# Performance work log

Hardware: AMD Instinct MI355X
Metric: run time of the kernel (lower is better)

The kernel has to match this reference:

```python
import jax, jax.numpy as jnp
import numpy as np
from jax import lax

BOS = 0
B, T, U = 8, 256, 64
IN, ENC_H, DEC_H, P, J, V = 80, 512, 512, 512, 512, 1024


def lstm_layer(x, Wih, Whh, b):
    """PyTorch-style LSTM layer. x: [B,T,I]; Wih: [4H,I]; Whh: [4H,H]; b: [4H]."""
    Bn = x.shape[0]
    H = Whh.shape[1]
    xp = jnp.einsum('bti,gi->btg', x, Wih) + b  # precompute input projections [B,T,4H]
    h0 = jnp.zeros((Bn, H), x.dtype)

    def step(carry, xt):
        h, c = carry
        g = xt + h @ Whh.T
        i, f, gg, o = jnp.split(g, 4, axis=-1)
        c = jax.nn.sigmoid(f) * c + jax.nn.sigmoid(i) * jnp.tanh(gg)
        h = jax.nn.sigmoid(o) * jnp.tanh(c)
        return (h, c), h

    _, hs = lax.scan(step, (h0, h0), xp.transpose(1, 0, 2))
    return hs.transpose(1, 0, 2)  # [B,T,H]


def setup_inputs() -> dict:
    key = jax.random.key(0)
    ks = jax.random.split(key, 20)
    s = 0.04  # ~1/sqrt(H) init scale
    inp = {
        'xs': jax.random.normal(ks[0], (B, T, IN), jnp.float32),
        'ys': jax.random.randint(ks[1], (B, U), 0, V),
        # encoder LSTM layer 0 / 1
        'enc_Wih0': jax.random.normal(ks[2], (4 * ENC_H, IN), jnp.float32) * s,
        'enc_Whh0': jax.random.normal(ks[3], (4 * ENC_H, ENC_H), jnp.float32) * s,
        'enc_b0': jnp.zeros((4 * ENC_H,), jnp.float32),
        'enc_Wih1': jax.random.normal(ks[4], (4 * ENC_H, ENC_H), jnp.float32) * s,
        'enc_Whh1': jax.random.normal(ks[5], (4 * ENC_H, ENC_H), jnp.float32) * s,
        'enc_b1': jnp.zeros((4 * ENC_H,), jnp.float32),
        'enc_projW': jax.random.normal(ks[6], (P, ENC_H), jnp.float32) * s,
        'enc_projb': jnp.zeros((P,), jnp.float32),
        # decoder
        'embed': jax.random.normal(ks[7], (V, DEC_H), jnp.float32) * s,
        'dec_Wih': jax.random.normal(ks[8], (4 * DEC_H, DEC_H), jnp.float32) * s,
        'dec_Whh': jax.random.normal(ks[9], (4 * DEC_H, DEC_H), jnp.float32) * s,
        'dec_b': jnp.zeros((4 * DEC_H,), jnp.float32),
        'dec_projW': jax.random.normal(ks[10], (P, DEC_H), jnp.float32) * s,
        'dec_projb': jnp.zeros((P,), jnp.float32),
        # joint MLP: Linear(2P -> J), Tanh, Linear(J -> V)
        'jW1': jax.random.normal(ks[11], (J, 2 * P), jnp.float32) * s,
        'jb1': jnp.zeros((J,), jnp.float32),
        'jW2': jax.random.normal(ks[12], (V, J), jnp.float32) * s,
        'jb2': jnp.zeros((V,), jnp.float32),
    }
    return inp


def reference(xs, ys, enc_Wih0, enc_Whh0, enc_b0, enc_Wih1, enc_Whh1, enc_b1,
              enc_projW, enc_projb, embed, dec_Wih, dec_Whh, dec_b,
              dec_projW, dec_projb, jW1, jb1, jW2, jb2):
    # Encoder: 2-layer LSTM + projection
    h = lstm_layer(xs, enc_Wih0, enc_Whh0, enc_b0)
    h = lstm_layer(h, enc_Wih1, enc_Whh1, enc_b1)
    h_enc = h @ enc_projW.T + enc_projb  # [B,T,P]

    # Decoder: BOS pad, embed, 1-layer LSTM + projection
    ys_p = jnp.pad(ys, ((0, 0), (1, 0)), constant_values=BOS)  # [B,U+1]
    e = embed[ys_p]
    hd = lstm_layer(e, dec_Wih, dec_Whh, dec_b)
    h_dec = hd @ dec_projW.T + dec_projb  # [B,U+1,P]

    # Joint: cat([h_enc,h_dec]) @ W1.T == h_enc @ W1[:,:P].T + h_dec @ W1[:,P:].T
    pre_enc = jnp.einsum('btp,jp->btj', h_enc, jW1[:, :P])
    pre_dec = jnp.einsum('bup,jp->buj', h_dec, jW1[:, P:])
    z = jnp.tanh(pre_enc[:, :, None, :] + pre_dec[:, None, :, :] + jb1)  # [B,T,U+1,J]
    logits = jnp.einsum('btuj,vj->btuv', z, jW2) + jb2  # [B,T,U+1,V]
    return logits
```

## Files before the change

### kernel.cpp

```cpp
#include <hip/hip_runtime.h>


typedef _Float16 f16;
typedef _Float16 f16x8 __attribute__((ext_vector_type(8)));
typedef float f32x4 __attribute__((ext_vector_type(4)));
using u32 = unsigned int;

#define BB   8
#define TT   256
#define UU1  65
#define HH   512
#define G4   2048
#define PP   512
#define JJ   512
#define VV   1024
#define SENT 0xFFFFFFFFu

#define LOADX(p)     __hip_atomic_load((p), __ATOMIC_RELAXED, __HIP_MEMORY_SCOPE_AGENT)
#define STOREX(p, v) __hip_atomic_store((p), (v), __ATOMIC_RELAXED, __HIP_MEMORY_SCOPE_AGENT)

static __device__ __forceinline__ u32 packf16(float a, float b) {
  f16 ha = (f16)a, hb = (f16)b;
  unsigned short ua = __builtin_bit_cast(unsigned short, ha);
  unsigned short ub = __builtin_bit_cast(unsigned short, hb);
  return (u32)ua | ((u32)ub << 16);
}
static __device__ __forceinline__ float sigm(float x) {
  x = fminf(30.f, fmaxf(-30.f, x));
  return __builtin_amdgcn_rcpf(1.f + __expf(-x));
}
static __device__ __forceinline__ float ftanh(float x) {
  x = fminf(15.f, fmaxf(-15.f, x));
  float t = __expf(2.f * x);
  return (t - 1.f) * __builtin_amdgcn_rcpf(t + 1.f);
}

__global__ void k_init(u32* __restrict__ p, int n, int z1, int z2) {
  int i = blockIdx.x * 256 + threadIdx.x;
  if (i >= n) return;
  bool z = (i < 2048) | ((u32)(i - z1) < 2048u) | ((u32)(i - z2) < 2048u);
  p[i] = z ? 0u : SENT;
}

struct CastSeg { const float* s; f16* d; int n4; };
struct CastArgs { CastSeg seg[10]; };
__global__ void k_cast_all(CastArgs a, int total4) {
  int i = blockIdx.x * 256 + threadIdx.x;
  if (i >= total4) return;
  int k = 0, off = i;
  while (off >= a.seg[k].n4) { off -= a.seg[k].n4; ++k; }
  const float4 v = *(const float4*)(a.seg[k].s + (size_t)off * 4);
  uint2 p; p.x = packf16(v.x, v.y); p.y = packf16(v.z, v.w);
  *(uint2*)(a.seg[k].d + (size_t)off * 4) = p;
}

__global__ void k_embed(const int* __restrict__ ys, const float* __restrict__ emb,
                        float* __restrict__ e) {
  int row = blockIdx.x;
  int b = row / UU1, u = row % UU1;
  int idx = (u == 0) ? 0 : ys[b * (UU1 - 1) + (u - 1)];
  const float4* s = (const float4*)(emb + (size_t)idx * HH);
  float4* d = (float4*)(e + (size_t)row * HH);
  d[threadIdx.x] = s[threadIdx.x];
}

__global__ void k_biasdot(const float* __restrict__ jW1, const float* __restrict__ encPb,
                          const float* __restrict__ dPb, const float* __restrict__ jb1,
                          float* __restrict__ bce, float* __restrict__ bcd) {
  int j = blockIdx.x * 256 + threadIdx.x;
  if (j >= 512) return;
  const float* rowE = jW1 + (size_t)j * 1024;
  const float* rowD = rowE + 512;
  float s1 = 0.f, s2 = 0.f;
  for (int p = 0; p < 512; p += 4) {
    float4 a = *(const float4*)(rowE + p), b = *(const float4*)(encPb + p);
    s1 += a.x * b.x + a.y * b.y + a.z * b.z + a.w * b.w;
    float4 c = *(const float4*)(rowD + p), d = *(const float4*)(dPb + p);
    s2 += c.x * d.x + c.y * d.y + c.z * d.z + c.w * d.w;
  }
  bce[j] = s1; bcd[j] = s2 + jb1[j];
}

__global__ __launch_bounds__(256) void k_gemm(
    const float* __restrict__ A, const f16* __restrict__ B,
    const float* __restrict__ bias, float* __restrict__ C,
    int M, int N, int K, int lda, int ldb) {
  __shared__ f16 As[128][72];
  __shared__ f16 Bs[128][72];
  int tid = threadIdx.x;
  int mb = blockIdx.y * 128, nb = blockIdx.x * 128;
  int wave = tid >> 6, lane = tid & 63;
  int wm = wave >> 1, wn = wave & 1;
  int rowa = lane & 15, kg = lane >> 4;
  f32x4 acc[4][4] = {};
  for (int k0 = 0; k0 < K; k0 += 64) {
    for (int idx = tid; idx < 2048; idx += 256) {
      int r = idx >> 4, cq = idx & 15;
      int gm = mb + r, gk = k0 + cq * 4;
      float4 v = make_float4(0.f, 0.f, 0.f, 0.f);
      if (gm < M && gk + 3 < K) v = *(const float4*)(A + (size_t)gm * lda + gk);
      uint2 p; p.x = packf16(v.x, v.y); p.y = packf16(v.z, v.w);
      *(uint2*)&As[r][cq * 4] = p;
    }
    for (int idx = tid; idx < 1024; idx += 256) {
      int r = idx >> 3, c8 = idx & 7;
      int gn = nb + r, gk = k0 + c8 * 8;
      uint4 v = make_uint4(0u, 0u, 0u, 0u);
      if (gn < N && gk + 7 < K) v = *(const uint4*)(B + (size_t)gn * ldb + gk);
      *(uint4*)&Bs[r][c8 * 8] = v;
    }
    __syncthreads();
#pragma unroll
    for (int kf = 0; kf < 2; ++kf) {
      f16x8 af[4], bf[4];
#pragma unroll
      for (int mt = 0; mt < 4; ++mt)
        af[mt] = *(const f16x8*)&As[wm * 64 + mt * 16 + rowa][kf * 32 + kg * 8];
#pragma unroll
      for (int nt = 0; nt < 4; ++nt)
        bf[nt] = *(const f16x8*)&Bs[wn * 64 + nt * 16 + rowa][kf * 32 + kg * 8];
#pragma unroll
      for (int mt = 0; mt < 4; ++mt)
#pragma unroll
        for (int nt = 0; nt < 4; ++nt)
          acc[mt][nt] = __builtin_amdgcn_mfma_f32_16x16x32_f16(af[mt], bf[nt], acc[mt][nt], 0, 0, 0);
    }
    __syncthreads();
  }
#pragma unroll
  for (int nt = 0; nt < 4; ++nt) {
    int gn = nb + wn * 64 + nt * 16 + rowa;
    float bv = bias ? bias[gn] : 0.f;
#pragma unroll
    for (int mt = 0; mt < 4; ++mt)
#pragma unroll
      for (int r = 0; r < 4; ++r) {
        int gm = mb + wm * 64 + mt * 16 + kg * 4 + r;
        if (gm < M) C[(size_t)gm * N + gn] = acc[mt][nt][r] + bv;
      }
  }
}

__global__ __launch_bounds__(256) void k_gemmT(
    const float* __restrict__ A, int lda, const f16* __restrict__ B2,
    f16* __restrict__ C16) {
  __shared__ f16 As[128][72];
  __shared__ f16 Bs[128][72];
  int tid = threadIdx.x;
  int mb = blockIdx.y * 128, nb = blockIdx.x * 128;
  int wave = tid >> 6, lane = tid & 63;
  int wm = wave >> 1, wn = wave & 1;
  int rowa = lane & 15, kg = lane >> 4;
  f32x4 acc[4][4] = {};
  for (int k0 = 0; k0 < 512; k0 += 64) {
    for (int idx = tid; idx < 2048; idx += 256) {
      int r = idx >> 4, cq = idx & 15;
      float4 v = *(const float4*)(A + (size_t)(mb + r) * lda + k0 + cq * 4);
      uint2 p; p.x = packf16(v.x, v.y); p.y = packf16(v.z, v.w);
      *(uint2*)&As[r][cq * 4] = p;
    }
    for (int idx = tid; idx < 1024; idx += 256) {
      int r = idx >> 4, c8 = idx & 15;
      uint4 v = *(const uint4*)(B2 + (size_t)(k0 + r) * 512 + nb + c8 * 8);
      f16 tmp[8]; *(uint4*)tmp = v;
#pragma unroll
      for (int e = 0; e < 8; ++e) Bs[c8 * 8 + e][r] = tmp[e];
    }
    __syncthreads();
#pragma unroll
    for (int kf = 0; kf < 2; ++kf) {
      f16x8 af[4], bf[4];
#pragma unroll
      for (int mt = 0; mt < 4; ++mt)
        af[mt] = *(const f16x8*)&As[wm * 64 + mt * 16 + rowa][kf * 32 + kg * 8];
#pragma unroll
      for (int nt = 0; nt < 4; ++nt)
        bf[nt] = *(const f16x8*)&Bs[wn * 64 + nt * 16 + rowa][kf * 32 + kg * 8];
#pragma unroll
      for (int mt = 0; mt < 4; ++mt)
#pragma unroll
        for (int nt = 0; nt < 4; ++nt)
          acc[mt][nt] = __builtin_amdgcn_mfma_f32_16x16x32_f16(af[mt], bf[nt], acc[mt][nt], 0, 0, 0);
    }
    __syncthreads();
  }
#pragma unroll
  for (int nt = 0; nt < 4; ++nt) {
    int gn = nb + wn * 64 + nt * 16 + rowa;
#pragma unroll
    for (int mt = 0; mt < 4; ++mt)
#pragma unroll
      for (int r = 0; r < 4; ++r) {
        int gm = mb + wm * 64 + mt * 16 + kg * 4 + r;
        C16[(size_t)gm * 512 + gn] = (f16)acc[mt][nt][r];
      }
  }
}

template <int NW>
static __device__ __forceinline__ void poll_batch(const u32* const* p, u32* vv) {
#pragma unroll
  for (int k = 0; k < NW; ++k) vv[k] = LOADX(p[k]);
  int gd = 0;
  while (++gd < (1 << 18)) {
    bool any = false;
#pragma unroll
    for (int k = 0; k < NW; ++k) any = any | (vv[k] == SENT);
    if (!any) break;
    __builtin_amdgcn_s_sleep(4);
#pragma unroll
    for (int k = 0; k < NW; ++k)
      if (vv[k] == SENT) vv[k] = LOADX(p[k]);
  }
}
static __device__ __forceinline__ void guard_spin(const u32* gp) {
  u32 v = LOADX(gp);
  int gd = 0;
  while (v == SENT && ++gd < (1 << 18)) {
    __builtin_amdgcn_s_sleep(2);
    v = LOADX(gp);
  }
}

static __device__ __forceinline__ void lstm_16(
    int wg, const float* __restrict__ xp, const f16* __restrict__ Whh,
    u32* __restrict__ hseq,
    float* __restrict__ hs, int S) {
  extern __shared__ char smem[];
  f16 (*W)[520] = (f16(*)[520])smem;
  f16 (*H)[520] = (f16(*)[520])(smem + 133120);
  float (*gat)[8][36] = (float(*)[8][36])(smem + 133120 + 8320);
  const int tid = threadIdx.x;
  const int u0 = wg * 32;
  const int wave = tid >> 6, lane = tid & 63;
  const int rowa = lane & 15, kg = lane >> 4;
  const int b = lane >> 3, ju = lane & 7;
  const int uglob = u0 + wave * 8 + ju;

  for (int idx = tid; idx < 128 * 64; idx += 256) {
    int r = idx >> 6, ck = idx & 63;
    int w = r >> 5, g = (r >> 3) & 3, u = r & 7;
    uint4 v = *(const uint4*)(Whh + ((size_t)(g * 512 + u0 + w * 8 + u)) * 512 + ck * 8);
    *(uint4*)&W[r][ck * 8] = v;
  }
  __syncthreads();

  float c = 0.f;
  for (int t = 0; t < S; ++t) {
    const u32* hb = hseq + (size_t)t * 2048;
    if (tid < 16) guard_spin(hb + tid * 16);
    __syncthreads();

    size_t xpo = ((size_t)b * S + t) * (size_t)G4 + uglob;
    float xi = xp[xpo], xf = xp[xpo + 512], xg = xp[xpo + 1024], xo = xp[xpo + 1536];

    const u32* ptr[8];
    u32 vv[8];
#pragma unroll
    for (int k = 0; k < 8; ++k) ptr[k] = hb + ((tid + k * 256) >> 8) * 256 + ((tid + k * 256) & 255);
    poll_batch<8>(ptr, vv);
#pragma unroll
    for (int k = 0; k < 8; ++k) {
      int idx = tid + k * 256;
      ((u32*)H)[(idx >> 8) * 260 + (idx & 255)] = vv[k];
    }
    __syncthreads();

    f32x4 acc0 = {0.f, 0.f, 0.f, 0.f}, acc1 = {0.f, 0.f, 0.f, 0.f};
#pragma unroll
    for (int kf = 0; kf < 16; ++kf) {
      f16x8 af = {};
      if (rowa < 8) af = *(const f16x8*)&H[rowa][kf * 32 + kg * 8];
      f16x8 b0 = *(const f16x8*)&W[wave * 32 + rowa][kf * 32 + kg * 8];
      f16x8 b1 = *(const f16x8*)&W[wave * 32 + 16 + rowa][kf * 32 + kg * 8];
      acc0 = __builtin_amdgcn_mfma_f32_16x16x32_f16(af, b0, acc0, 0, 0, 0);
      acc1 = __builtin_amdgcn_mfma_f32_16x16x32_f16(af, b1, acc1, 0, 0, 0);
    }
    if (kg < 2) {
#pragma unroll
      for (int r = 0; r < 4; ++r) {
        gat[wave][kg * 4 + r][rowa] = acc0[r];
        gat[wave][kg * 4 + r][16 + rowa] = acc1[r];
      }
    }
    float gi = gat[wave][b][ju] + xi;
    float gf = gat[wave][b][8 + ju] + xf;
    float gg = gat[wave][b][16 + ju] + xg;
    float go = gat[wave][b][24 + ju] + xo;
    c = sigm(gf) * c + sigm(gi) * ftanh(gg);
    float h = sigm(go) * ftanh(c);

    float hn = __shfl_down(h, 1);
    if ((ju & 1) == 0)
      STOREX(hseq + (size_t)(t + 1) * 2048 + ((b * 512 + uglob) >> 1), packf16(h, hn));
    if (hs) hs[((size_t)b * S + t) * HH + uglob] = h;
  }
}

static __device__ __forceinline__ void lstm_l1(
    int wg, const float* __restrict__ gb, const f16* __restrict__ Wih,
    const f16* __restrict__ Whh, const u32* __restrict__ hin,
    u32* __restrict__ hseq, float* __restrict__ hs, int S) {
  extern __shared__ char smem[];
  f16 (*W)[1032] = (f16(*)[1032])smem;
  f16 (*H)[1032] = (f16(*)[1032])(smem + 132096);
  float (*gat)[8][20] = (float(*)[8][20])(smem + 132096 + 16512);
  const int tid = threadIdx.x;
  const int u0 = wg * 16;
  const int wave = tid >> 6, lane = tid & 63;
  const int rowa = lane & 15, kg = lane >> 4;
  const int b = lane >> 2, ju = lane & 3;
  const int uglob = u0 + wave * 4 + ju;

  for (int idx = tid; idx < 64 * 64; idx += 256) {
    int r = idx >> 6, ck = idx & 63;
    int w = r >> 4, g = (r >> 2) & 3, u = r & 3;
    size_t grow = (size_t)(g * 512 + u0 + w * 4 + u) * 512;
    *(uint4*)&W[r][ck * 8]       = *(const uint4*)(Whh + grow + ck * 8);
    *(uint4*)&W[r][512 + ck * 8] = *(const uint4*)(Wih + grow + ck * 8);
  }
  float gbi = 0.f, gbf = 0.f, gbg = 0.f, gbo = 0.f;
  if (lane < 32) {
    gbi = gb[uglob]; gbf = gb[512 + uglob];
    gbg = gb[1024 + uglob]; gbo = gb[1536 + uglob];
  }
  __syncthreads();

  float c = 0.f;
  for (int t = 0; t < S; ++t) {
    const u32* hbS = hseq + (size_t)t * 2048;
    const u32* hbU = hin + (size_t)(t + 1) * 2048;
    if (tid < 32)       guard_spin(hbS + tid * 8);
    else if (tid < 48)  guard_spin(hbU + (tid - 32) * 16);
    __syncthreads();
    const u32* ptr[16];
    u32 vv[16];
#pragma unroll
    for (int k = 0; k < 8; ++k) {
      int idx = tid + k * 256;
      int r = idx >> 8, cu = idx & 255;
      ptr[k] = hbS + r * 256 + cu;
      ptr[k + 8] = hbU + r * 256 + cu;
    }
    poll_batch<16>(ptr, vv);
#pragma unroll
    for (int k = 0; k < 8; ++k) {
      int idx = tid + k * 256;
      int r = idx >> 8, cu = idx & 255;
      ((u32*)H)[r * 516 + cu] = vv[k];
      ((u32*)H)[r * 516 + 256 + cu] = vv[k + 8];
    }
    __syncthreads();

    f32x4 accA = {0.f, 0.f, 0.f, 0.f}, accB = {0.f, 0.f, 0.f, 0.f};
#pragma unroll
    for (int kf = 0; kf < 16; ++kf) {
      f16x8 afA = {}, afB = {};
      if (rowa < 8) {
        afA = *(const f16x8*)&H[rowa][kf * 32 + kg * 8];
        afB = *(const f16x8*)&H[rowa][(kf + 16) * 32 + kg * 8];
      }
      f16x8 bfA = *(const f16x8*)&W[wave * 16 + rowa][kf * 32 + kg * 8];
      f16x8 bfB = *(const f16x8*)&W[wave * 16 + rowa][(kf + 16) * 32 + kg * 8];
      accA = __builtin_amdgcn_mfma_f32_16x16x32_f16(afA, bfA, accA, 0, 0, 0);
      accB = __builtin_amdgcn_mfma_f32_16x16x32_f16(afB, bfB, accB, 0, 0, 0);
    }
    if (kg < 2) {
#pragma unroll
      for (int r = 0; r < 4; ++r) gat[wave][kg * 4 + r][rowa] = accA[r] + accB[r];
    }
    if (lane < 32) {
      float gi = gat[wave][b][ju]      + gbi;
      float gf = gat[wave][b][4 + ju]  + gbf;
      float gg = gat[wave][b][8 + ju]  + gbg;
      float go = gat[wave][b][12 + ju] + gbo;
      c = sigm(gf) * c + sigm(gi) * ftanh(gg);
      float h = sigm(go) * ftanh(c);
      float hn = __shfl_down(h, 1);
      if ((ju & 1) == 0)
        STOREX(hseq + (size_t)(t + 1) * 2048 + (b * 256 + (uglob >> 1)), packf16(h, hn));
      hs[((size_t)b * S + t) * HH + uglob] = h;
    }
  }
}

__global__ __launch_bounds__(256, 1) void k_lstm3(
    const float* xp0, const f16* Whh0, u32* hseq0,
    const float* b1, const f16* Wih1, const f16* Whh1, u32* hseq1, float* h1s,
    const float* xpd, const f16* Whhd, u32* hseqD, float* hds) {
  int g = blockIdx.x;
  if (g < 16)      lstm_16(g, xp0, Whh0, hseq0, nullptr, TT);
  else if (g < 48) lstm_l1(g - 16, b1, Wih1, Whh1, hseq0, hseq1, h1s, TT);
  else             lstm_16(g - 48, xpd, Whhd, hseqD, hds, UU1);
}

__global__ __launch_bounds__(512, 4) void k_joint(
    const float* __restrict__ pre_enc,
    const float* __restrict__ pre_dec,
    const f16* __restrict__ jW2,
    const float* __restrict__ jb2,
    float* __restrict__ out) {
  extern __shared__ char smem[];
  f16 (*Z)[520] = (f16(*)[520])smem;
  f16 (*Bs)[72] = (f16(*)[72])(smem + 66560);
  int tid = threadIdx.x;
  int m0 = blockIdx.x * 64;
  {
    int r = tid >> 3, q = tid & 7;
    int m = m0 + r;
    int bb = m / (TT * UU1);
    int rem = m % (TT * UU1);
    int t = rem / UU1, u = rem % UU1;
    const float* pe = pre_enc + ((size_t)bb * TT + t) * JJ + q * 64;
    const float* pd = pre_dec + ((size_t)bb * UU1 + u) * JJ + q * 64;
    for (int i = 0; i < 64; i += 8) {
      float4 e0 = *(const float4*)(pe + i);
      float4 e1 = *(const float4*)(pe + i + 4);
      float4 d0 = *(const float4*)(pd + i);
      float4 d1 = *(const float4*)(pd + i + 4);
      float z0 = ftanh(e0.x + d0.x), z1 = ftanh(e0.y + d0.y);
      float z2 = ftanh(e0.z + d0.z), z3 = ftanh(e0.w + d0.w);
      float z4 = ftanh(e1.x + d1.x), z5 = ftanh(e1.y + d1.y);
      float z6 = ftanh(e1.z + d1.z), z7 = ftanh(e1.w + d1.w);
      uint4 p; p.x = packf16(z0, z1); p.y = packf16(z2, z3);
      p.z = packf16(z4, z5); p.w = packf16(z6, z7);
      *(uint4*)&Z[r][q * 64 + i] = p;
    }
  }
  const int wave = tid >> 6, lane = tid & 63;
  const int wm = wave >> 2, wn = wave & 3;
  const int rowa = lane & 15, kg = lane >> 4;
  const int r8 = tid >> 3, c8 = tid & 7;

  uint4 nreg = *(const uint4*)(jW2 + (size_t)r8 * JJ + c8 * 8);

  f32x4 acc[2] = {};
  for (int it = 0; it < 128; ++it) {
    const int vc = it >> 3, ks = it & 7;
    __syncthreads();
    *(uint4*)&Bs[r8][c8 * 8] = nreg;
    if (it < 127) {
      int nvc = (it + 1) >> 3, nks = (it + 1) & 7;
      nreg = *(const uint4*)(jW2 + (size_t)(nvc * 64 + r8) * JJ + nks * 64 + c8 * 8);
    }
    __syncthreads();
#pragma unroll
    for (int kf = 0; kf < 2; ++kf) {
      int zo = ks * 64 + kf * 32 + kg * 8;
      f16x8 af  = *(const f16x8*)&Bs[wn * 16 + rowa][kf * 32 + kg * 8];
      f16x8 bf0 = *(const f16x8*)&Z[wm * 32 + rowa][zo];
      f16x8 bf1 = *(const f16x8*)&Z[wm * 32 + 16 + rowa][zo];
      acc[0] = __builtin_amdgcn_mfma_f32_16x16x32_f16(af, bf0, acc[0], 0, 0, 0);
      acc[1] = __builtin_amdgcn_mfma_f32_16x16x32_f16(af, bf1, acc[1], 0, 0, 0);
    }
    if (ks == 7) {
      int v = vc * 64 + wn * 16 + kg * 4;
      float4 bv = *(const float4*)(jb2 + v);
#pragma unroll
      for (int mt = 0; mt < 2; ++mt) {
        int m = m0 + wm * 32 + mt * 16 + rowa;
        f32x4 st;
        st[0] = acc[mt][0] + bv.x;
        st[1] = acc[mt][1] + bv.y;
        st[2] = acc[mt][2] + bv.z;
        st[3] = acc[mt][3] + bv.w;
        __builtin_nontemporal_store(st, (f32x4*)(out + (size_t)m * VV + v));
        acc[mt] = (f32x4){0.f, 0.f, 0.f, 0.f};
      }
    }
  }
}

extern "C" void kernel_launch(void* const* d_in, const int* in_sizes, int n_in,
                              void* d_out, int out_size, void* d_ws, size_t ws_size,
                              hipStream_t stream) {
  const float* xs    = (const float*)d_in[0];
  const int*   ys    = (const int*)d_in[1];
  const float* Wih0  = (const float*)d_in[2];
  const float* Whh0  = (const float*)d_in[3];
  const float* b0    = (const float*)d_in[4];
  const float* Wih1  = (const float*)d_in[5];
  const float* Whh1  = (const float*)d_in[6];
  const float* b1    = (const float*)d_in[7];
  const float* encPW = (const float*)d_in[8];
  const float* encPb = (const float*)d_in[9];
  const float* embed = (const float*)d_in[10];
  const float* dWih  = (const float*)d_in[11];
  const float* dWhh  = (const float*)d_in[12];
  const float* db    = (const float*)d_in[13];
  const float* dPW   = (const float*)d_in[14];
  const float* dPb   = (const float*)d_in[15];
  const float* jW1   = (const float*)d_in[16];
  const float* jb1   = (const float*)d_in[17];
  const float* jW2   = (const float*)d_in[18];
  const float* jb2   = (const float*)d_in[19];
  float* out = (float*)d_out;

  char* base = (char*)d_ws;
  size_t off = 0;
  auto alc = [&](size_t bytes) -> char* {
    char* p = base + off;
    off = (off + bytes + 255) & ~(size_t)255;
    return p;
  };
  f16* Wih0h = (f16*)alc((size_t)2048 * 80 * 2);
  f16* Whh0h = (f16*)alc((size_t)2048 * 512 * 2);
  f16* Wih1h = (f16*)alc((size_t)2048 * 512 * 2);
  f16* Whh1h = (f16*)alc((size_t)2048 * 512 * 2);
  f16* dWihh = (f16*)alc((size_t)2048 * 512 * 2);
  f16* dWhhh = (f16*)alc((size_t)2048 * 512 * 2);
  f16* ePWh  = (f16*)alc((size_t)512 * 512 * 2);
  f16* dPWh  = (f16*)alc((size_t)512 * 512 * 2);
  f16* jW2h  = (f16*)alc((size_t)1024 * 512 * 2);
  f16* Wceh  = (f16*)alc((size_t)512 * 512 * 2);
  f16* Wcdh  = (f16*)alc((size_t)512 * 512 * 2);
  float* bce  = (float*)alc((size_t)512 * 4);
  float* bcd  = (float*)alc((size_t)512 * 4);
  float* e    = (float*)alc((size_t)520 * 512 * 4);
  float* xp0  = (float*)alc((size_t)2048 * 2048 * 4);
  float* xpd  = (float*)alc((size_t)520 * 2048 * 4);
  float* h1s  = (float*)alc((size_t)2048 * 512 * 4);
  float* hds  = (float*)alc((size_t)520 * 512 * 4);
  float* penc = (float*)alc((size_t)2048 * 512 * 4);
  float* pdec = (float*)alc((size_t)520 * 512 * 4);
  u32* hseq0 = (u32*)alc((size_t)(TT + 1) * 2048 * 4);
  u32* hseq1 = (u32*)alc((size_t)(TT + 1) * 2048 * 4);
  u32* hseqD = (u32*)alc((size_t)(UU1 + 1) * 2048 * 4);
  if (off > ws_size) return;

  {
    int n = (int)(((TT + 1) * 2 + (UU1 + 1)) * 2048);
    int z1 = (int)(hseq1 - hseq0), z2 = (int)(hseqD - hseq0);
    k_init<<<dim3((n + 255) / 256), dim3(256), 0, stream>>>(hseq0, n, z1, z2);
  }
  {
    CastArgs ca = {};
    auto seg = [&](int i, const float* s, f16* d, size_t n) {
      ca.seg[i].s = s; ca.seg[i].d = d; ca.seg[i].n4 = (int)(n / 4);
    };
    seg(0, Wih0, Wih0h, (size_t)2048 * 80);
    seg(1, Whh0, Whh0h, (size_t)2048 * 512);
    seg(2, Wih1, Wih1h, (size_t)2048 * 512);
    seg(3, Whh1, Whh1h, (size_t)2048 * 512);
    seg(4, dWih, dWihh, (size_t)2048 * 512);
    seg(5, dWhh, dWhhh, (size_t)2048 * 512);
    seg(6, encPW, ePWh, (size_t)512 * 512);
    seg(7, dPW, dPWh, (size_t)512 * 512);
    seg(8, jW2, jW2h, (size_t)1024 * 512);
    int total4 = 0;
    for (int i = 0; i < 9; ++i) total4 += ca.seg[i].n4;
    k_cast_all<<<dim3((total4 + 255) / 256), dim3(256), 0, stream>>>(ca, total4);
  }
  k_gemmT<<<dim3(4, 4), dim3(256), 0, stream>>>(jW1, 1024, ePWh, Wceh);
  k_gemmT<<<dim3(4, 4), dim3(256), 0, stream>>>(jW1 + 512, 1024, dPWh, Wcdh);
  k_biasdot<<<dim3(2), dim3(256), 0, stream>>>(jW1, encPb, dPb, jb1, bce, bcd);

  k_embed<<<dim3(520), dim3(128), 0, stream>>>(ys, embed, e);

  auto gemm = [&](const float* A, const f16* B, const float* bias, float* C,
                  int M, int N, int K, int lda, int ldb) {
    k_gemm<<<dim3(N / 128, (M + 127) / 128), dim3(256), 0, stream>>>(
        A, B, bias, C, M, N, K, lda, ldb);
  };

  gemm(xs, Wih0h, b0, xp0, 2048, 2048, 80, 80, 80);
  gemm(e, dWihh, db, xpd, 520, 2048, 512, 512, 512);

  k_lstm3<<<dim3(64), dim3(256), 151168, stream>>>(
      xp0, Whh0h, hseq0,
      b1, Wih1h, Whh1h, hseq1, h1s,
      xpd, dWhhh, hseqD, hds);

  gemm(h1s, Wceh, bce, penc, 2048, 512, 512, 512, 512);
  gemm(hds, Wcdh, bcd, pdec, 520, 512, 512, 512, 512);

  k_joint<<<dim3(2080), dim3(512), 75776, stream>>>(penc, pdec, jW2h, jb2, out);
}
```

Baseline: 1.426 ms.

## Hold joint W2 fragments in registers instead of staging through LDS

The joint GEMM kernel no longer stages jW2 tiles through shared memory with two barriers per k-step. Each wave now loads its 16-row slice of W2 for the full K directly into registers, computes all 64 M rows against it, and prefetches the next 128-column chunk while storing results. This removes the per-iteration barriers and LDS traffic for W2, at the cost of heavy register use (16 f16x8 fragments per lane), which may lower occupancy. The guard spin-wait sleep in the LSTM is also shortened to poll more often.

```diff
diff --git a/kernel.cpp b/kernel.cpp
--- a/kernel.cpp
+++ b/kernel.cpp
@@ -217,7 +217,7 @@
   u32 v = LOADX(gp);
   int gd = 0;
   while (v == SENT && ++gd < (1 << 18)) {
-    __builtin_amdgcn_s_sleep(2);
+    __builtin_amdgcn_s_sleep(1);
     v = LOADX(gp);
   }
 }
@@ -400,11 +400,19 @@
     const f16* __restrict__ jW2,
     const float* __restrict__ jb2,
     float* __restrict__ out) {
-  extern __shared__ char smem[];
-  f16 (*Z)[520] = (f16(*)[520])smem;
-  f16 (*Bs)[72] = (f16(*)[72])(smem + 66560);
+  __shared__ f16 Z[64][520];
   int tid = threadIdx.x;
   int m0 = blockIdx.x * 64;
+  const int wave = tid >> 6, lane = tid & 63;
+  const int rowa = lane & 15, kg = lane >> 4;
+
+  f16x8 af[16];
+  {
+    const f16* wb = jW2 + (size_t)(wave * 16 + rowa) * JJ + kg * 8;
+#pragma unroll
+    for (int kf = 0; kf < 16; ++kf) af[kf] = *(const f16x8*)(wb + kf * 32);
+  }
+
   {
     int r = tid >> 3, q = tid & 7;
     int m = m0 + r;
@@ -427,46 +435,35 @@
       *(uint4*)&Z[r][q * 64 + i] = p;
     }
   }
-  const int wave = tid >> 6, lane = tid & 63;
-  const int wm = wave >> 2, wn = wave & 3;
-  const int rowa = lane & 15, kg = lane >> 4;
-  const int r8 = tid >> 3, c8 = tid & 7;
-
-  uint4 nreg = *(const uint4*)(jW2 + (size_t)r8 * JJ + c8 * 8);
-
-  f32x4 acc[2] = {};
-  for (int it = 0; it < 128; ++it) {
-    const int vc = it >> 3, ks = it & 7;
-    __syncthreads();
-    *(uint4*)&Bs[r8][c8 * 8] = nreg;
-    if (it < 127) {
-      int nvc = (it + 1) >> 3, nks = (it + 1) & 7;
-      nreg = *(const uint4*)(jW2 + (size_t)(nvc * 64 + r8) * JJ + nks * 64 + c8 * 8);
-    }
-    __syncthreads();
-#pragma unroll
-    for (int kf = 0; kf < 2; ++kf) {
-      int zo = ks * 64 + kf * 32 + kg * 8;
-      f16x8 af  = *(const f16x8*)&Bs[wn * 16 + rowa][kf * 32 + kg * 8];
-      f16x8 bf0 = *(const f16x8*)&Z[wm * 32 + rowa][zo];
-      f16x8 bf1 = *(const f16x8*)&Z[wm * 32 + 16 + rowa][zo];
-      acc[0] = __builtin_amdgcn_mfma_f32_16x16x32_f16(af, bf0, acc[0], 0, 0, 0);
-      acc[1] = __builtin_amdgcn_mfma_f32_16x16x32_f16(af, bf1, acc[1], 0, 0, 0);
-    }
-    if (ks == 7) {
-      int v = vc * 64 + wn * 16 + kg * 4;
-      float4 bv = *(const float4*)(jb2 + v);
-#pragma unroll
-      for (int mt = 0; mt < 2; ++mt) {
-        int m = m0 + wm * 32 + mt * 16 + rowa;
-        f32x4 st;
-        st[0] = acc[mt][0] + bv.x;
-        st[1] = acc[mt][1] + bv.y;
-        st[2] = acc[mt][2] + bv.z;
-        st[3] = acc[mt][3] + bv.w;
-        __builtin_nontemporal_store(st, (f32x4*)(out + (size_t)m * VV + v));
-        acc[mt] = (f32x4){0.f, 0.f, 0.f, 0.f};
+  __syncthreads();
+
+  for (int ch = 0; ch < 8; ++ch) {
+    f32x4 acc[4] = {};
+#pragma unroll
+    for (int kf = 0; kf < 16; ++kf) {
+      int zo = kf * 32 + kg * 8;
+#pragma unroll
+      for (int mt = 0; mt < 4; ++mt) {
+        f16x8 bf = *(const f16x8*)&Z[mt * 16 + rowa][zo];
+        acc[mt] = __builtin_amdgcn_mfma_f32_16x16x32_f16(af[kf], bf, acc[mt], 0, 0, 0);
       }
+    }
+    int v = ch * 128 + wave * 16 + kg * 4;
+    if (ch < 7) {
+      const f16* wb = jW2 + (size_t)((ch + 1) * 128 + wave * 16 + rowa) * JJ + kg * 8;
+#pragma unroll
+      for (int kf = 0; kf < 16; ++kf) af[kf] = *(const f16x8*)(wb + kf * 32);
+    }
+    float4 bv = *(const float4*)(jb2 + v);
+#pragma unroll
+    for (int mt = 0; mt < 4; ++mt) {
+      int m = m0 + mt * 16 + rowa;
+      f32x4 st;
+      st[0] = acc[mt][0] + bv.x;
+      st[1] = acc[mt][1] + bv.y;
+      st[2] = acc[mt][2] + bv.z;
+      st[3] = acc[mt][3] + bv.w;
+      __builtin_nontemporal_store(st, (f32x4*)(out + (size_t)m * VV + v));
     }
   }
 }
@@ -574,5 +571,5 @@
   gemm(h1s, Wceh, bce, penc, 2048, 512, 512, 512, 512);
   gemm(hds, Wcdh, bcd, pdec, 520, 512, 512, 512, 512);
 
-  k_joint<<<dim3(2080), dim3(512), 75776, stream>>>(penc, pdec, jW2h, jb2, out);
-}
+  k_joint<<<dim3(2080), dim3(512), 0, stream>>>(penc, pdec, jW2h, jb2, out);
+}
```

New measurement: 2.573 ms. +80.4%, slower.

## Halve joint kernel M-tile, stage output through LDS for coalesced stores

Applied to the files above, without the earlier changes.

The joint kernel's row tile drops from 64 to 32, so each wave now issues one MFMA per k-slice instead of two, the grid doubles, and launch bounds ask for 6 blocks per CU using static shared memory. Results are staged through a shared Cs buffer so each thread writes a contiguous row segment, giving coalesced nontemporal stores in place of scattered column-fragment stores. The aim is higher occupancy and better write coalescing for the large output. The cost is reloading the jW2 tiles twice as often per output row and an extra barrier in each epilogue. The LSTM guard spin sleep is also shortened.

```diff
diff --git a/kernel.cpp b/kernel.cpp
--- a/kernel.cpp
+++ b/kernel.cpp
@@ -217,7 +217,7 @@
   u32 v = LOADX(gp);
   int gd = 0;
   while (v == SENT && ++gd < (1 << 18)) {
-    __builtin_amdgcn_s_sleep(2);
+    __builtin_amdgcn_s_sleep(1);
     v = LOADX(gp);
   }
 }
@@ -394,26 +394,33 @@
   else             lstm_16(g - 48, xpd, Whhd, hseqD, hds, UU1);
 }
 
-__global__ __launch_bounds__(512, 4) void k_joint(
+__global__ __launch_bounds__(512, 6) void k_joint(
     const float* __restrict__ pre_enc,
     const float* __restrict__ pre_dec,
     const f16* __restrict__ jW2,
     const float* __restrict__ jb2,
     float* __restrict__ out) {
-  extern __shared__ char smem[];
-  f16 (*Z)[520] = (f16(*)[520])smem;
-  f16 (*Bs)[72] = (f16(*)[72])(smem + 66560);
+  __shared__ f16 Z[32][520];
+  __shared__ f16 Bs[64][72];
+  __shared__ float Cs[32][68];
   int tid = threadIdx.x;
-  int m0 = blockIdx.x * 64;
+  int m0 = blockIdx.x * 32;
+  const int wave = tid >> 6, lane = tid & 63;
+  const int mt = wave >> 2, vt = wave & 3;
+  const int rowa = lane & 15, kg = lane >> 4;
+  const int r8 = tid >> 3, c8 = tid & 7;
+
+  uint4 nreg = *(const uint4*)(jW2 + (size_t)r8 * JJ + c8 * 8);
+
   {
-    int r = tid >> 3, q = tid & 7;
+    int r = tid >> 4, q = tid & 15;
     int m = m0 + r;
     int bb = m / (TT * UU1);
     int rem = m % (TT * UU1);
     int t = rem / UU1, u = rem % UU1;
-    const float* pe = pre_enc + ((size_t)bb * TT + t) * JJ + q * 64;
-    const float* pd = pre_dec + ((size_t)bb * UU1 + u) * JJ + q * 64;
-    for (int i = 0; i < 64; i += 8) {
+    const float* pe = pre_enc + ((size_t)bb * TT + t) * JJ + q * 32;
+    const float* pd = pre_dec + ((size_t)bb * UU1 + u) * JJ + q * 32;
+    for (int i = 0; i < 32; i += 8) {
       float4 e0 = *(const float4*)(pe + i);
       float4 e1 = *(const float4*)(pe + i + 4);
       float4 d0 = *(const float4*)(pd + i);
@@ -424,17 +431,11 @@
       float z6 = ftanh(e1.z + d1.z), z7 = ftanh(e1.w + d1.w);
       uint4 p; p.x = packf16(z0, z1); p.y = packf16(z2, z3);
       p.z = packf16(z4, z5); p.w = packf16(z6, z7);
-      *(uint4*)&Z[r][q * 64 + i] = p;
-    }
-  }
-  const int wave = tid >> 6, lane = tid & 63;
-  const int wm = wave >> 2, wn = wave & 3;
-  const int rowa = lane & 15, kg = lane >> 4;
-  const int r8 = tid >> 3, c8 = tid & 7;
-
-  uint4 nreg = *(const uint4*)(jW2 + (size_t)r8 * JJ + c8 * 8);
-
-  f32x4 acc[2] = {};
+      *(uint4*)&Z[r][q * 32 + i] = p;
+    }
+  }
+
+  f32x4 acc = {};
   for (int it = 0; it < 128; ++it) {
     const int vc = it >> 3, ks = it & 7;
     __syncthreads();
@@ -446,27 +447,23 @@
     __syncthreads();
 #pragma unroll
     for (int kf = 0; kf < 2; ++kf) {
-      int zo = ks * 64 + kf * 32 + kg * 8;
-      f16x8 af  = *(const f16x8*)&Bs[wn * 16 + rowa][kf * 32 + kg * 8];
-      f16x8 bf0 = *(const f16x8*)&Z[wm * 32 + rowa][zo];
-      f16x8 bf1 = *(const f16x8*)&Z[wm * 32 + 16 + rowa][zo];
-      acc[0] = __builtin_amdgcn_mfma_f32_16x16x32_f16(af, bf0, acc[0], 0, 0, 0);
-      acc[1] = __builtin_amdgcn_mfma_f32_16x16x32_f16(af, bf1, acc[1], 0, 0, 0);
+      f16x8 af = *(const f16x8*)&Bs[vt * 16 + rowa][kf * 32 + kg * 8];
+      f16x8 bf = *(const f16x8*)&Z[mt * 16 + rowa][ks * 64 + kf * 32 + kg * 8];
+      acc = __builtin_amdgcn_mfma_f32_16x16x32_f16(af, bf, acc, 0, 0, 0);
     }
     if (ks == 7) {
-      int v = vc * 64 + wn * 16 + kg * 4;
-      float4 bv = *(const float4*)(jb2 + v);
-#pragma unroll
-      for (int mt = 0; mt < 2; ++mt) {
-        int m = m0 + wm * 32 + mt * 16 + rowa;
-        f32x4 st;
-        st[0] = acc[mt][0] + bv.x;
-        st[1] = acc[mt][1] + bv.y;
-        st[2] = acc[mt][2] + bv.z;
-        st[3] = acc[mt][3] + bv.w;
-        __builtin_nontemporal_store(st, (f32x4*)(out + (size_t)m * VV + v));
-        acc[mt] = (f32x4){0.f, 0.f, 0.f, 0.f};
-      }
+      int vl = vt * 16 + kg * 4;
+      float4 bv = *(const float4*)(jb2 + vc * 64 + vl);
+      f32x4 st;
+      st[0] = acc[0] + bv.x; st[1] = acc[1] + bv.y;
+      st[2] = acc[2] + bv.z; st[3] = acc[3] + bv.w;
+      *(f32x4*)&Cs[mt * 16 + rowa][vl] = st;
+      acc = (f32x4){0.f, 0.f, 0.f, 0.f};
+      __syncthreads();
+      int m = tid >> 4, vi = (tid & 15) * 4;
+      f32x4 row = *(const f32x4*)&Cs[m][vi];
+      __builtin_nontemporal_store(row,
+          (f32x4*)(out + (size_t)(m0 + m) * VV + vc * 64 + vi));
     }
   }
 }
@@ -574,5 +571,5 @@
   gemm(h1s, Wceh, bce, penc, 2048, 512, 512, 512, 512);
   gemm(hds, Wcdh, bcd, pdec, 520, 512, 512, 512, 512);
 
-  k_joint<<<dim3(2080), dim3(512), 75776, stream>>>(penc, pdec, jW2h, jb2, out);
-}
+  k_joint<<<dim3(4160), dim3(512), 0, stream>>>(penc, pdec, jW2h, jb2, out);
+}
```

After: 1.428 ms. About the same (+0.1%).
